# Performance work log

Measured on AMD Instinct MI355X. Metric: run time of the kernel, lower is better.

Reference implementation:

```python
import jax, jax.numpy as jnp
import numpy as np

N_NODES = 100000
N_EDGES = 600000
N_FEAT = 166
HID = 128


def _ln(x, g, b, eps=1e-5):
    m = x.mean(-1, keepdims=True)
    v = ((x - m) ** 2).mean(-1, keepdims=True)
    return (x - m) * jax.lax.rsqrt(v + eps) * g + b


def _gcn(h, row, col, em, W, b, n):
    # PyG GCNConv with add_self_loops=True; em is a 0/1 edge mask (recent/history split)
    hl = h @ W.T  # [N,H], PyG internal Linear has no bias
    deg = jax.ops.segment_sum(em, col, num_segments=n) + 1.0  # +1 for self loop
    dis = jax.lax.rsqrt(deg)
    coef = em * dis[row] * dis[col]
    agg = jax.ops.segment_sum(hl[row] * coef[:, None], col, num_segments=n)
    agg = agg + hl * (dis * dis)[:, None]  # self-loop message
    return agg + b


def setup_inputs():
    key = jax.random.key(0)
    ks = jax.random.split(key, 16)
    f32 = jnp.float32
    H = HID
    z = lambda *s: jnp.zeros(s, f32)
    nrm = lambda k, s, sc=0.05: jax.random.normal(k, s, f32) * sc
    return {
        "x": jax.random.normal(ks[0], (N_NODES, N_FEAT), f32),
        "edge_index": jax.random.randint(ks[1], (2, N_EDGES), 0, N_NODES, jnp.int32),
        "timestamps": jax.random.uniform(ks[2], (N_EDGES,), f32),
        "memory": nrm(ks[3], (N_NODES, H), 0.1),
        "W_in": nrm(ks[4], (H, N_FEAT)), "b_in": z(H),
        "W_time": nrm(ks[5], (H, 1)), "b_time": z(H),
        "W_ih": nrm(ks[6], (3 * H, H)), "W_hh": nrm(ks[7], (3 * H, H)),
        "b_ih": z(3 * H), "b_hh": z(3 * H),
        "W_gr": nrm(ks[8], (H, H)), "b_gr": z(H),
        "W_gh": nrm(ks[9], (H, H)), "b_gh": z(H),
        "ln_pa_g": jnp.ones((H,), f32), "ln_pa_b": z(H),
        "Wv": nrm(ks[10], (H, H)), "bv": z(H),
        "Wo": nrm(ks[11], (H, H)), "bo": z(H),
        "ln_at_g": jnp.ones((H,), f32), "ln_at_b": z(H),
        "W1": nrm(ks[12], (64, H)), "b1": z(64),
        "W2": nrm(ks[13], (2, 64)), "b2": z(2),
    }


def reference(x, edge_index, timestamps, memory, W_in, b_in, W_time, b_time,
              W_ih, W_hh, b_ih, b_hh, W_gr, b_gr, W_gh, b_gh,
              ln_pa_g, ln_pa_b, Wv, bv, Wo, bo, ln_at_g, ln_at_b,
              W1, b1, W2, b2):
    n = x.shape[0]
    row, col = edge_index[0], edge_index[1]
    # input projection + scatter-max temporal encoding
    h = x @ W_in.T + b_in
    nt = jnp.maximum(jax.ops.segment_max(timestamps, col, num_segments=n), 0.0)  # torch_scatter max inits at 0
    tmin, tmax = nt.min(), nt.max()
    nt = jnp.where(tmax > tmin, (nt - tmin) / (tmax - tmin + 1e-8), nt)
    h = h + nt[:, None] * W_time[:, 0] + b_time  # Linear(1, H)
    h = jax.nn.relu(h)
    h = h + memory
    # gather -> GRUCell -> scatter memory update for nodes touched by any edge
    upd = jnp.zeros((n,), bool).at[edge_index.reshape(-1)].set(True)
    gi = h @ W_ih.T + b_ih
    gh = memory @ W_hh.T + b_hh
    ir, iz, ic = jnp.split(gi, 3, axis=1)
    hr, hz, hc = jnp.split(gh, 3, axis=1)
    r = jax.nn.sigmoid(ir + hr)
    z = jax.nn.sigmoid(iz + hz)
    c = jnp.tanh(ic + r * hc)
    new_memory = jnp.where(upd[:, None], (1.0 - z) * c + z * memory, memory)
    # split edges by median timestamp, two GCN paths
    med = jnp.median(timestamps)
    m_rec = (timestamps >= med).astype(h.dtype)
    h_rec = _gcn(h, row, col, m_rec, W_gr, b_gr, n)
    h_his = _gcn(h, row, col, 1.0 - m_rec, W_gh, b_gh, n)
    # multi-path aggregation with softmax over per-path mean scores
    stacked = jnp.stack([h_rec, h_his], axis=1)  # [N,2,H]
    w = jax.nn.softmax(stacked.mean(-1), axis=-1)[..., None]
    h = _ln((stacked * w).sum(1), ln_pa_g, ln_pa_b)
    # anomaly attention: L=S=1 per "batch" element, so softmax over one key == 1
    # => attended = out_proj(v_proj(x)); query path cancels exactly
    attended = (h @ Wv.T + bv) @ Wo.T + bo
    h = _ln(h + attended, ln_at_g, ln_at_b)
    # classifier (eval mode: dropout = identity)
    logits = jax.nn.relu(h @ W1.T + b1) @ W2.T + b2
    return logits, new_memory
```

## Files before the change

### kernel.cpp

```cpp
#include <hip/hip_runtime.h>

#define NN 100000
#define NE 600000
#define NF 166
#define NH 128
#define NNH 12800000

enum { EPI_PLAIN = 0, EPI_RELU = 2, EPI_H = 3, EPI_HEAD = 4, EPI_ATTLN = 5 };

typedef short bf16x8 __attribute__((ext_vector_type(8)));
typedef float f32x16 __attribute__((ext_vector_type(16)));
typedef _Float16 f16x2 __attribute__((ext_vector_type(2)));
typedef _Float16 f16x4 __attribute__((ext_vector_type(4)));
typedef _Float16 f16x8 __attribute__((ext_vector_type(8)));

__device__ __forceinline__ unsigned short f2bf(float f) {
  unsigned u = __float_as_uint(f);
  u += 0x7fffu + ((u >> 16) & 1u);
  return (unsigned short)(u >> 16);
}

__device__ __forceinline__ unsigned short f2h(float f) {
  return __builtin_bit_cast(unsigned short, (_Float16)f);
}

__device__ __forceinline__ void gl_lds16(const void* g, void* l) {
  __builtin_amdgcn_global_load_lds((__attribute__((address_space(1))) void*)(void*)g,
                                   (__attribute__((address_space(3))) void*)l, 16, 0, 0);
}

template<int EPI, int OUTK, bool BIAS2, bool CONC, bool DUALA, bool F16, int NT>
__launch_bounds__(256)
__global__ void mgemm(const unsigned short* __restrict__ A, int lda,
                      const unsigned short* __restrict__ A2,
                      const unsigned short* __restrict__ W, int ldw,
                      float* __restrict__ C, int ldc,
                      unsigned short* __restrict__ Cb, int ldcb,
                      int K, int M,
                      const float* __restrict__ bias, const float* __restrict__ bias2,
                      const float* __restrict__ wtv, const float* __restrict__ ntv,
                      const float* __restrict__ mem, const int* __restrict__ scal)
{
  __shared__ unsigned short As[128 * 64];
  __shared__ unsigned short Bs[NT * 32 * 64];
  const int tid = threadIdx.x;
  const int wave = tid >> 6, lane = tid & 63;
  const int row0 = blockIdx.y * 128, col0 = blockIdx.x * NT * 32;
  if (DUALA && blockIdx.x) { A = A2; bias = bias2; }
  const int hi = lane >> 5, l5 = lane & 31, l3 = lane & 7;
  f32x16 acc[NT] = {};

  for (int k0 = 0; k0 < K; k0 += 64) {
    const unsigned short* Asrc = A;
    int kk = k0;
    if (CONC && k0 >= 128) { Asrc = A2; kk = k0 - 128; }
    __syncthreads();
#pragma unroll
    for (int q = 0; q < 4; ++q) {
      int id = q * 256 + tid;
      int r = id >> 3, cch = id & 7;
      int sw = ((cch ^ (r & 7)) << 3);
      int gr = row0 + r; if (gr > NN - 1) gr = NN - 1;
      gl_lds16(Asrc + (size_t)gr * lda + kk + sw, &As[(q * 256 + wave * 64) * 8]);
    }
#pragma unroll
    for (int q = 0; q < NT; ++q) {
      int id = q * 256 + tid;
      int r = id >> 3, cch = id & 7;
      int sw = ((cch ^ (r & 7)) << 3);
      int gm = col0 + r; if (gm > M - 1) gm = M - 1;
      gl_lds16(W + (size_t)gm * ldw + k0 + sw, &Bs[(q * 256 + wave * 64) * 8]);
    }
    __syncthreads();
#pragma unroll
    for (int s = 0; s < 4; ++s) {
      int slot8 = (((s * 2 + hi) ^ l3) << 3);
      bf16x8 a = *(const bf16x8*)&As[(wave * 32 + l5) * 64 + slot8];
#pragma unroll
      for (int t = 0; t < NT; ++t) {
        bf16x8 b = *(const bf16x8*)&Bs[(t * 32 + l5) * 64 + slot8];
        if (F16)
          acc[t] = __builtin_amdgcn_mfma_f32_32x32x16_f16(
              __builtin_bit_cast(f16x8, a), __builtin_bit_cast(f16x8, b), acc[t], 0, 0, 0);
        else
          acc[t] = __builtin_amdgcn_mfma_f32_32x32x16_bf16(a, b, acc[t], 0, 0, 0);
      }
    }
  }

  float tmin = 0.f, tmax = 0.f;
  if (EPI == EPI_H) { tmin = __int_as_float(scal[5]); tmax = __int_as_float(scal[6]); }
  float bc[NT], wc[NT], b2c[NT];
#pragma unroll
  for (int t = 0; t < NT; ++t) {
    int gcol = col0 + t * 32 + l5;
    int bcol = DUALA ? (gcol & 127) : gcol;
    bc[t] = bias ? bias[bcol] : 0.f;
    if (BIAS2) bc[t] += bias2[gcol];
    if (EPI == EPI_H)     { bc[t] += bias2[gcol]; wc[t] = wtv[gcol]; }
    if (EPI == EPI_ATTLN) { wc[t] = wtv[gcol]; b2c[t] = bias2[gcol]; }
  }
#pragma unroll
  for (int rg = 0; rg < 16; ++rg) {
    int lr = (rg & 3) + 8 * (rg >> 2) + 4 * hi;
    int grow = row0 + wave * 32 + lr;
    if (grow >= NN) continue;
    float ntn = 0.f;
    if (EPI == EPI_H) {
      ntn = ntv[grow];
      if (tmax > tmin) ntn = (ntn - tmin) / (tmax - tmin + 1e-8f);
    }
    float hv[NT];
#pragma unroll
    for (int t = 0; t < NT; ++t) {
      float v = acc[t][rg] + bc[t];
      if (EPI == EPI_RELU || EPI == EPI_HEAD) v = fmaxf(v, 0.f);
      if (EPI == EPI_H) {
        v += ntn * wc[t];
        v = fmaxf(v, 0.f);
        float mv = mem[(size_t)grow * NH + (col0 + t * 32 + l5)];
        v += mv;
        ((unsigned short*)C)[(size_t)grow * NH + (col0 + t * 32 + l5)] = f2bf(mv);
      }
      hv[t] = v;
    }
    if (EPI == EPI_ATTLN) {
      const _Float16* h2r = (const _Float16*)mem;
      float s = 0.f;
#pragma unroll
      for (int t = 0; t < NT; ++t) {
        hv[t] += (float)h2r[(size_t)grow * NH + (col0 + t * 32 + l5)];
        s += hv[t];
      }
#pragma unroll
      for (int d = 1; d < 32; d <<= 1) s += __shfl_xor(s, d);
      float mean = s * (1.f / 128.f);
      float var = 0.f;
#pragma unroll
      for (int t = 0; t < NT; ++t) { hv[t] -= mean; var += hv[t] * hv[t]; }
#pragma unroll
      for (int d = 1; d < 32; d <<= 1) var += __shfl_xor(var, d);
      float rstd = rsqrtf(var * (1.f / 128.f) + 1e-5f);
#pragma unroll
      for (int t = 0; t < NT; ++t) hv[t] = hv[t] * rstd * wc[t] + b2c[t];
    }
    if (EPI == EPI_HEAD) {
      float p0 = hv[0] * wtv[l5]      + hv[1] * wtv[32 + l5];
      float p1 = hv[0] * wtv[64 + l5] + hv[1] * wtv[96 + l5];
#pragma unroll
      for (int d = 1; d < 32; d <<= 1) { p0 += __shfl_xor(p0, d); p1 += __shfl_xor(p1, d); }
      if (l5 == 0) {
        C[(size_t)grow * 2]     = p0 + bias2[0];
        C[(size_t)grow * 2 + 1] = p1 + bias2[1];
      }
    } else {
#pragma unroll
      for (int t = 0; t < NT; ++t) {
        int gcol = col0 + t * 32 + l5;
        if (OUTK == 1) C[(size_t)grow * ldc + gcol] = hv[t];
        if (OUTK == 2) Cb[(size_t)grow * ldcb + gcol] = f2bf(hv[t]);
        if (OUTK == 3) Cb[(size_t)grow * ldcb + gcol] = f2h(hv[t]);
      }
    }
  }
}

__global__ void conv_x(const float* __restrict__ x, unsigned short* __restrict__ xb)
{
  int i = blockIdx.x * 256 + threadIdx.x;
  if (i >= NN * 192) return;
  int n = i / 192, c = i - n * 192;
  xb[i] = (c < NF) ? f2bf(x[n * NF + c]) : (unsigned short)0;
}

__global__ void conv_w(const float* __restrict__ Wi, const float* __restrict__ Wih,
                       const float* __restrict__ Whh, const float* __restrict__ Wgr,
                       const float* __restrict__ Wgh, const float* __restrict__ Wv,
                       const float* __restrict__ Wo, const float* __restrict__ W1,
                       unsigned short* __restrict__ wb)
{
  int i = blockIdx.x * 256 + threadIdx.x;
  if (i >= 196608) return;
  float v;
  if (i < 24576)       { int r = i / 192, c = i - r * 192; v = (c < NF) ? Wi[r * NF + c] : 0.f; }
  else if (i < 90112)  { int j = i - 24576; int r = j >> 8, c = j & 255;
                         v = (c < 128) ? Wih[r * 128 + c] : Whh[r * 128 + (c - 128)]; }
  else if (i < 122880) { int j = i - 90112; int r = j >> 7, c = j & 127;
                         v = (r < 128) ? Wih[(256 + r) * 128 + c] : Whh[(128 + r) * 128 + c]; }
  else if (i < 139264) v = Wgr[i - 122880];
  else if (i < 155648) v = Wgh[i - 139264];
  else if (i < 172032) v = Wv[i - 155648];
  else if (i < 188416) v = Wo[i - 172032];
  else                 v = W1[i - 188416];
  wb[i] = f2bf(v);
}

__global__ void compose_att(const float* __restrict__ Wv, const float* __restrict__ Wo,
                            const float* __restrict__ bv, const float* __restrict__ bo,
                            _Float16* __restrict__ wout, float* __restrict__ bout)
{
  int i = blockIdx.x * 256 + threadIdx.x;
  if (i >= 16384) return;
  int r = i >> 7, c = i & 127;
  float s = 0.f;
  for (int k = 0; k < 128; ++k) s = fmaf(Wo[r * 128 + k], Wv[k * 128 + c], s);
  wout[i] = (_Float16)s;
  if (c == 0) {
    float t = bo[r];
    for (int k = 0; k < 128; ++k) t = fmaf(Wo[r * 128 + k], bv[k], t);
    bout[r] = t;
  }
}

__device__ __forceinline__ int ts_bin(float t) {
  int b = (int)(t * 65536.0f);
  return b > 65535 ? 65535 : (b < 0 ? 0 : b);
}

__global__ void edge_pass1(const int* __restrict__ row, const int* __restrict__ col,
                           const float* __restrict__ ts,
                           float* nt, int* upd, int* cnt_all, int* hist1)
{
  int e = blockIdx.x * 256 + threadIdx.x;
  if (e >= NE) return;
  int r = row[e], c = col[e];
  float t = ts[e];
  atomicMax((int*)(nt + c), __float_as_int(t));
  upd[r] = 1; upd[c] = 1;
  atomicAdd(cnt_all + c, 1);
  atomicAdd(hist1 + ts_bin(t), 1);
}

__global__ void node_minmax(const float* __restrict__ nt, int* scal)
{
  int i = blockIdx.x * 256 + threadIdx.x;
  float v = (i < NN) ? nt[i] : nt[0];
  float vmin = v, vmax = v;
#pragma unroll
  for (int d = 1; d < 64; d <<= 1) {
    vmin = fminf(vmin, __shfl_xor(vmin, d));
    vmax = fmaxf(vmax, __shfl_xor(vmax, d));
  }
  __shared__ float smin[4], smax[4];
  int lane = threadIdx.x & 63, w = threadIdx.x >> 6;
  if (lane == 0) { smin[w] = vmin; smax[w] = vmax; }
  __syncthreads();
  if (threadIdx.x == 0) {
    float a = fminf(fminf(smin[0], smin[1]), fminf(smin[2], smin[3]));
    float b = fmaxf(fmaxf(smax[0], smax[1]), fmaxf(smax[2], smax[3]));
    atomicMin(scal + 5, __float_as_int(a));
    atomicMax(scal + 6, __float_as_int(b));
  }
}

__global__ void scan_hist1(const int* __restrict__ hist, int* scal)
{
  const int K1 = 299999, K2 = 300000;
  __shared__ int sums[256];
  __shared__ int pre[257];
  int t = threadIdx.x;
  int s = 0;
  for (int i = 0; i < 256; ++i) s += hist[t * 256 + i];
  sums[t] = s;
  __syncthreads();
  if (t == 0) { int run = 0; for (int i = 0; i < 256; ++i) { pre[i] = run; run += sums[i]; } pre[256] = run; }
  __syncthreads();
  int base = pre[t], nexts = base + sums[t];
  if (K1 >= base && K1 < nexts) {
    int run = base;
    for (int i = 0; i < 256; ++i) {
      int cv = hist[t * 256 + i];
      if (K1 < run + cv) { scal[0] = t * 256 + i; scal[1] = run; break; }
      run += cv;
    }
  }
  if (K2 >= base && K2 < nexts) {
    int run = base;
    for (int i = 0; i < 256; ++i) {
      int cv = hist[t * 256 + i];
      if (K2 < run + cv) { scal[2] = t * 256 + i; scal[3] = run; break; }
      run += cv;
    }
  }
}

#define CAND_CAP 4096
__global__ void collect_cand(const float* __restrict__ ts, const int* __restrict__ scal,
                             float* cand1, float* cand2, int* ccnt)
{
  int e = blockIdx.x * 256 + threadIdx.x;
  if (e >= NE) return;
  float t = ts[e];
  int b = ts_bin(t);
  if (b == scal[0]) {
    int s = atomicAdd(ccnt + 0, 1);
    if (s < CAND_CAP) cand1[s] = t;
  }
  if (b == scal[2]) {
    int s = atomicAdd(ccnt + 1, 1);
    if (s < CAND_CAP) cand2[s] = t;
  }
}

__global__ void select_med(const float* __restrict__ c1, const float* __restrict__ c2,
                           const int* __restrict__ ccnt, int* scal)
{
  __shared__ float res[2];
  for (int which = 0; which < 2; ++which) {
    const float* c = which ? c2 : c1;
    int m = ccnt[which]; if (m > CAND_CAP) m = CAND_CAP;
    int rank = which ? (300000 - scal[3]) : (299999 - scal[1]);
    for (int i = threadIdx.x; i < m; i += 256) {
      float v = c[i];
      int less = 0, eq = 0;
      for (int j = 0; j < m; ++j) { float w = c[j]; less += (w < v); eq += (w == v); }
      if (less <= rank && rank < less + eq) res[which] = v;
    }
  }
  __syncthreads();
  if (threadIdx.x == 0)
    ((float*)scal)[4] = 0.5f * (res[0] + res[1]);
}

__global__ void csr_scan1(const int* __restrict__ cnt, int* loc, int* bsum)
{
  __shared__ int s[256];
  int t = threadIdx.x;
  int i = blockIdx.x * 256 + t;
  int v = (i < NN) ? cnt[i] : 0;
  s[t] = v;
  __syncthreads();
  for (int d = 1; d < 256; d <<= 1) {
    int add = (t >= d) ? s[t - d] : 0;
    __syncthreads();
    s[t] += add;
    __syncthreads();
  }
  if (i < NN) loc[i] = s[t] - v;
  if (t == 255) bsum[blockIdx.x] = s[255];
}

__global__ void csr_scan2(int* bsum, int nb)
{
  if (threadIdx.x == 0) {
    int run = 0;
    for (int i = 0; i < nb; ++i) { int v = bsum[i]; bsum[i] = run; run += v; }
  }
}

__global__ void csr_scan3(const int* __restrict__ loc, const int* __restrict__ bsum,
                          int* off, int* fillpos)
{
  int i = blockIdx.x * 256 + threadIdx.x;
  if (i < NN) {
    int o = loc[i] + bsum[i >> 8];
    off[i] = o;
    fillpos[i] = o;
  }
  if (i == 0) off[NN] = NE;
}

__global__ void csr_fill(const int* __restrict__ row, const int* __restrict__ col,
                         const float* __restrict__ ts, const int* __restrict__ scal,
                         int* fillpos, int* elist, int* cnt_rec)
{
  int e = blockIdx.x * 256 + threadIdx.x;
  if (e >= NE) return;
  int c = col[e], r = row[e];
  int rec = (ts[e] >= __int_as_float(scal[4])) ? 1 : 0;
  if (rec) atomicAdd(cnt_rec + c, 1);
  int slot = atomicAdd(fillpos + c, 1);
  elist[slot] = r | (rec << 31);
}

__global__ void node_dis(const int* __restrict__ cnt_all, const int* __restrict__ cnt_rec,
                         float* dr, float* dh)
{
  int n = blockIdx.x * 256 + threadIdx.x;
  if (n >= NN) return;
  int ca = cnt_all[n], cr = cnt_rec[n];
  dr[n] = rsqrtf((float)cr + 1.f);
  dh[n] = rsqrtf((float)(ca - cr) + 1.f);
}

__device__ __forceinline__ float gru1(float rp, float zp, float ic, float hc, float mv) {
  float r = 1.f / (1.f + expf(-rp));
  float z = 1.f / (1.f + expf(-zp));
  float c = tanhf(ic + r * hc);
  return (1.f - z) * c + z * mv;
}

__global__ void gru_kernel(const _Float16* __restrict__ RZ, const _Float16* __restrict__ ICHC,
                           const float* __restrict__ mem, const int* __restrict__ upd,
                           float* __restrict__ out)
{
  int idx = blockIdx.x * 256 + threadIdx.x;
  if (idx >= NN * 32) return;
  int n = idx >> 5, q = (idx & 31) << 2;
  size_t p128 = (size_t)n * 128 + q;
  size_t p256 = (size_t)n * 256 + q;
  float4 mv = *(const float4*)(mem + p128);
  float4 o = mv;
  if (upd[n]) {
    f16x4 rp = *(const f16x4*)(RZ + p256);
    f16x4 zp = *(const f16x4*)(RZ + p256 + 128);
    f16x4 ic = *(const f16x4*)(ICHC + p256);
    f16x4 hc = *(const f16x4*)(ICHC + p256 + 128);
    o.x = gru1((float)rp[0], (float)zp[0], (float)ic[0], (float)hc[0], mv.x);
    o.y = gru1((float)rp[1], (float)zp[1], (float)ic[1], (float)hc[1], mv.y);
    o.z = gru1((float)rp[2], (float)zp[2], (float)ic[2], (float)hc[2], mv.z);
    o.w = gru1((float)rp[3], (float)zp[3], (float)ic[3], (float)hc[3], mv.w);
  }
  *(float4*)(out + p128) = o;
}

__global__ void gather_combine(const int* __restrict__ off, const int* __restrict__ elist,
                               const float* __restrict__ dis_r, const float* __restrict__ dis_h,
                               const _Float16* __restrict__ hl2,
                               const float* __restrict__ bgr, const float* __restrict__ bgh,
                               const float* __restrict__ g, const float* __restrict__ b,
                               _Float16* __restrict__ h2)
{
  int n = blockIdx.x * 4 + (threadIdx.x >> 6);
  if (n >= NN) return;
  int lane = threadIdx.x & 63;
  int o0 = __builtin_amdgcn_readfirstlane(off[n]);
  int o1 = __builtin_amdgcn_readfirstlane(off[n + 1]);
  float dnr = dis_r[n], dnh = dis_h[n];
  float arx = 0.f, ary = 0.f, ahx = 0.f, ahy = 0.f;
  int j = o0;
  for (; j + 1 < o1; j += 2) {
    int p0 = __builtin_amdgcn_readfirstlane(elist[j]);
    int p1 = __builtin_amdgcn_readfirstlane(elist[j + 1]);
    int r0 = p0 & 0x7fffffff, r1 = p1 & 0x7fffffff;
    int c0 = ((unsigned)p0) >> 31, c1 = ((unsigned)p1) >> 31;
    float d0 = c0 ? dis_r[r0] : dis_h[r0];
    float d1 = c1 ? dis_r[r1] : dis_h[r1];
    f16x2 v0 = *(const f16x2*)(hl2 + (size_t)r0 * 256 + ((c0 ^ 1) << 7) + (lane << 1));
    f16x2 v1 = *(const f16x2*)(hl2 + (size_t)r1 * 256 + ((c1 ^ 1) << 7) + (lane << 1));
    float k0 = d0 * (c0 ? dnr : dnh);
    float k1 = d1 * (c1 ? dnr : dnh);
    if (c0) { arx = fmaf(k0, (float)v0[0], arx); ary = fmaf(k0, (float)v0[1], ary); }
    else    { ahx = fmaf(k0, (float)v0[0], ahx); ahy = fmaf(k0, (float)v0[1], ahy); }
    if (c1) { arx = fmaf(k1, (float)v1[0], arx); ary = fmaf(k1, (float)v1[1], ary); }
    else    { ahx = fmaf(k1, (float)v1[0], ahx); ahy = fmaf(k1, (float)v1[1], ahy); }
  }
  if (j < o1) {
    int p0 = __builtin_amdgcn_readfirstlane(elist[j]);
    int r0 = p0 & 0x7fffffff;
    int c0 = ((unsigned)p0) >> 31;
    float d0 = c0 ? dis_r[r0] : dis_h[r0];
    f16x2 v0 = *(const f16x2*)(hl2 + (size_t)r0 * 256 + ((c0 ^ 1) << 7) + (lane << 1));
    float k0 = d0 * (c0 ? dnr : dnh);
    if (c0) { arx = fmaf(k0, (float)v0[0], arx); ary = fmaf(k0, (float)v0[1], ary); }
    else    { ahx = fmaf(k0, (float)v0[0], ahx); ahy = fmaf(k0, (float)v0[1], ahy); }
  }
  f16x2 lr = *(const f16x2*)(hl2 + (size_t)n * 256 + (lane << 1));
  f16x2 lh = *(const f16x2*)(hl2 + (size_t)n * 256 + 128 + (lane << 1));
  float2 br = *(const float2*)(bgr + (lane << 1));
  float2 bh = *(const float2*)(bgh + (lane << 1));
  float rx = arx + (float)lr[0] * dnr * dnr + br.x;
  float ry = ary + (float)lr[1] * dnr * dnr + br.y;
  float hx = ahx + (float)lh[0] * dnh * dnh + bh.x;
  float hy = ahy + (float)lh[1] * dnh * dnh + bh.y;
  float sa = rx + ry, sc = hx + hy;
#pragma unroll
  for (int d = 1; d < 64; d <<= 1) { sa += __shfl_xor(sa, d); sc += __shfl_xor(sc, d); }
  float m0 = sa * (1.f / 128.f), m1 = sc * (1.f / 128.f);
  float mx = fmaxf(m0, m1);
  float e0 = expf(m0 - mx), e1 = expf(m1 - mx);
  float inv = 1.f / (e0 + e1);
  float w0 = e0 * inv, w1 = e1 * inv;
  float yx = w0 * rx + w1 * hx;
  float yy = w0 * ry + w1 * hy;
  float s = yx + yy;
#pragma unroll
  for (int d = 1; d < 64; d <<= 1) s += __shfl_xor(s, d);
  float mean = s * (1.f / 128.f);
  float dx = yx - mean, dy = yy - mean;
  float vv = dx * dx + dy * dy;
#pragma unroll
  for (int d = 1; d < 64; d <<= 1) vv += __shfl_xor(vv, d);
  float rstd = rsqrtf(vv * (1.f / 128.f) + 1e-5f);
  float2 gg = *(const float2*)(g + (lane << 1));
  float2 bb = *(const float2*)(b + (lane << 1));
  f16x2 o;
  o[0] = (_Float16)(dx * rstd * gg.x + bb.x);
  o[1] = (_Float16)(dy * rstd * gg.y + bb.y);
  *(f16x2*)(h2 + (size_t)n * NH + (lane << 1)) = o;
}

extern "C" void kernel_launch(void* const* d_in, const int* in_sizes, int n_in,
                              void* d_out, int out_size, void* d_ws, size_t ws_size,
                              hipStream_t stream)
{
  const float* x      = (const float*)d_in[0];
  const int*   ei     = (const int*)  d_in[1];
  const float* ts     = (const float*)d_in[2];
  const float* mem    = (const float*)d_in[3];
  const float* W_in   = (const float*)d_in[4];
  const float* b_in   = (const float*)d_in[5];
  const float* W_time = (const float*)d_in[6];
  const float* b_time = (const float*)d_in[7];
  const float* W_ih   = (const float*)d_in[8];
  const float* W_hh   = (const float*)d_in[9];
  const float* b_ih   = (const float*)d_in[10];
  const float* b_hh   = (const float*)d_in[11];
  const float* W_gr   = (const float*)d_in[12];
  const float* b_gr   = (const float*)d_in[13];
  const float* W_gh   = (const float*)d_in[14];
  const float* b_gh   = (const float*)d_in[15];
  const float* ln_pa_g= (const float*)d_in[16];
  const float* ln_pa_b= (const float*)d_in[17];
  const float* Wv     = (const float*)d_in[18];
  const float* bv     = (const float*)d_in[19];
  const float* Wo     = (const float*)d_in[20];
  const float* bo     = (const float*)d_in[21];
  const float* ln_at_g= (const float*)d_in[22];
  const float* ln_at_b= (const float*)d_in[23];
  const float* W1     = (const float*)d_in[24];
  const float* b1     = (const float*)d_in[25];
  const float* W2     = (const float*)d_in[26];
  const float* b2     = (const float*)d_in[27];

  const int* row = ei;
  const int* col = ei + NE;
  float* out_logits = (float*)d_out;
  float* out_mem    = (float*)d_out + NN * 2;

  float* ws = (float*)d_ws;
  unsigned short* hb   = (unsigned short*)(ws);
  _Float16* h2         = (_Float16*)(ws);
  unsigned short* xb   = (unsigned short*)(ws + 6400000);
  _Float16* rz         = (_Float16*)(ws + 6400000);
  unsigned short* rb   = (unsigned short*)(ws + 6400000);
  _Float16* ichc       = (_Float16*)(ws + 19200000);
  _Float16* hl2        = (_Float16*)(ws + 32000000);
  unsigned short* memb = (unsigned short*)(ws + 44800000);
  unsigned short* wb   = (unsigned short*)(ws + 51200000);
  float* nt            = ws + 51350000;
  float* dis_r         = ws + 51450000;
  float* dis_h         = ws + 51550000;
  int* cnt_all         = (int*)(ws + 51650000);
  int* cnt_rec         = (int*)(ws + 51750000);
  int* upd             = (int*)(ws + 51850000);
  int* scal            = (int*)(ws + 51950000);
  float* batt          = ws + 51960000;
  float* cand1         = ws + 51970000;
  float* cand2         = ws + 51980000;
  int* ccnt            = (int*)(ws + 51990000);
  int* hist1           = (int*)(ws + 52000000);
  int* off             = (int*)(ws + 52100000);
  int* fillpos         = (int*)(ws + 52250000);
  int* loc             = (int*)(ws + 52400000);
  int* bsum            = (int*)(ws + 52550000);
  int* elist           = (int*)(ws + 52600000);

  unsigned short* wb_in = wb;
  unsigned short* wb_rz = wb + 24576;
  unsigned short* wb_c  = wb + 90112;
  unsigned short* wb_gr = wb + 122880;
  unsigned short* wb_o  = wb + 172032;
  unsigned short* wb_1  = wb + 188416;

  hipMemsetAsync(nt,      0, NN * 4, stream);
  hipMemsetAsync(cnt_all, 0, NN * 4, stream);
  hipMemsetAsync(cnt_rec, 0, NN * 4, stream);
  hipMemsetAsync(upd,     0, NN * 4, stream);
  hipMemsetAsync(hist1,   0, 65536 * 4, stream);
  hipMemsetAsync(scal,    0, 16 * 4, stream);
  hipMemsetAsync(scal + 5,0x7f, 4, stream);
  hipMemsetAsync(ccnt,    0, 8, stream);

  const int eb  = (NE + 255) / 256;
  const int nb  = (NN + 255) / 256;
  dim3 blk(256);
  const unsigned gy = (NN + 127) / 128;

  edge_pass1  <<<eb, 256, 0, stream>>>(row, col, ts, nt, upd, cnt_all, hist1);
  node_minmax <<<nb, 256, 0, stream>>>(nt, scal);
  scan_hist1  <<<1, 256, 0, stream>>>(hist1, scal);
  collect_cand<<<eb, 256, 0, stream>>>(ts, scal, cand1, cand2, ccnt);
  select_med  <<<1, 256, 0, stream>>>(cand1, cand2, ccnt, scal);

  conv_w     <<<768, 256, 0, stream>>>(W_in, W_ih, W_hh, W_gr, W_gh, Wv, Wo, W1, wb);
  compose_att<<<64, 256, 0, stream>>>(Wv, Wo, bv, bo, (_Float16*)wb_o, batt);
  conv_x     <<<75000, 256, 0, stream>>>(x, xb);

  mgemm<EPI_H, 2, false, false, false, false, 4><<<dim3(1, gy), blk, 0, stream>>>(
      xb, 192, nullptr, wb_in, 192, (float*)memb, 0, hb, NH, 192, 128,
      b_in, b_time, W_time, nt, mem, scal);
  mgemm<EPI_PLAIN, 3, true, true, false, false, 8><<<dim3(1, gy), blk, 0, stream>>>(
      hb, NH, memb, wb_rz, 256, nullptr, 0, (unsigned short*)rz, 256, 256, 256,
      b_ih, b_hh, nullptr, nullptr, nullptr, nullptr);
  mgemm<EPI_PLAIN, 3, false, false, true, false, 4><<<dim3(2, gy), blk, 0, stream>>>(
      hb, NH, memb, wb_c, NH, nullptr, 0, (unsigned short*)ichc, 256, 128, 256,
      b_ih + 256, b_hh + 256, nullptr, nullptr, nullptr, nullptr);
  gru_kernel<<<(NN * 32) / 256, 256, 0, stream>>>(rz, ichc, mem, upd, out_mem);

  csr_scan1<<<nb, 256, 0, stream>>>(cnt_all, loc, bsum);
  csr_scan2<<<1, 64, 0, stream>>>(bsum, nb);
  csr_scan3<<<nb, 256, 0, stream>>>(loc, bsum, off, fillpos);
  csr_fill <<<eb, 256, 0, stream>>>(row, col, ts, scal, fillpos, elist, cnt_rec);
  node_dis <<<nb, 256, 0, stream>>>(cnt_all, cnt_rec, dis_r, dis_h);

  mgemm<EPI_PLAIN, 3, false, false, false, false, 8><<<dim3(1, gy), blk, 0, stream>>>(
      hb, NH, nullptr, wb_gr, NH, nullptr, 0, (unsigned short*)hl2, 256, 128, 256,
      nullptr, nullptr, nullptr, nullptr, nullptr, nullptr);

  gather_combine<<<(NN + 3) / 4, 256, 0, stream>>>(off, elist, dis_r, dis_h, hl2,
      b_gr, b_gh, ln_pa_g, ln_pa_b, h2);

  mgemm<EPI_ATTLN, 2, false, false, false, true, 4><<<dim3(1, gy), blk, 0, stream>>>(
      (const unsigned short*)h2, NH, nullptr, wb_o, NH, nullptr, 0, rb, NH, 128, 128,
      batt, ln_at_b, ln_at_g, nullptr, (const float*)h2, scal);

  mgemm<EPI_HEAD, 0, false, false, false, false, 2><<<dim3(1, gy), blk, 0, stream>>>(
      rb, NH, nullptr, wb_1, NH, out_logits, 0, nullptr, 0, 128, 64,
      b1, b2, W2, nullptr, nullptr, nullptr);

  (void)in_sizes; (void)n_in; (void)out_size; (void)ws_size;
}
```

Baseline: 758.2 us.

## Restructure edge preprocessing around CSR with block-local histograms and per-node scan

Replaces the 65536-bin global-atomic timestamp histogram with a 1024-bin histogram that each block builds in shared memory and writes out as a partial, reduced in one scan kernel. Median-candidate collection moves into the CSR fill pass, which also stores timestamps in CSR order. A new node_scan kernel then derives per-node max time, recent-edge counts, degree normalisers, the recent flag bits and the min/max reduction from the CSR segments. This removes several global-atomic passes and separate kernels. The coarser bins put more candidates into the quadratic select_med step. The upd flag array shrinks to bytes.

```diff
diff --git a/kernel.cpp b/kernel.cpp
--- a/kernel.cpp
+++ b/kernel.cpp
@@ -212,96 +212,56 @@
   }
 }
 
+#define NBIN 1024
+#define HBLK 256
 __device__ __forceinline__ int ts_bin(float t) {
-  int b = (int)(t * 65536.0f);
-  return b > 65535 ? 65535 : (b < 0 ? 0 : b);
-}
-
-__global__ void edge_pass1(const int* __restrict__ row, const int* __restrict__ col,
+  int b = (int)(t * (float)NBIN);
+  return b > NBIN - 1 ? NBIN - 1 : (b < 0 ? 0 : b);
+}
+
+__global__ void edge_count(const int* __restrict__ row, const int* __restrict__ col,
                            const float* __restrict__ ts,
-                           float* nt, int* upd, int* cnt_all, int* hist1)
-{
-  int e = blockIdx.x * 256 + threadIdx.x;
-  if (e >= NE) return;
-  int r = row[e], c = col[e];
-  float t = ts[e];
-  atomicMax((int*)(nt + c), __float_as_int(t));
-  upd[r] = 1; upd[c] = 1;
-  atomicAdd(cnt_all + c, 1);
-  atomicAdd(hist1 + ts_bin(t), 1);
-}
-
-__global__ void node_minmax(const float* __restrict__ nt, int* scal)
-{
-  int i = blockIdx.x * 256 + threadIdx.x;
-  float v = (i < NN) ? nt[i] : nt[0];
-  float vmin = v, vmax = v;
-#pragma unroll
-  for (int d = 1; d < 64; d <<= 1) {
-    vmin = fminf(vmin, __shfl_xor(vmin, d));
-    vmax = fmaxf(vmax, __shfl_xor(vmax, d));
-  }
-  __shared__ float smin[4], smax[4];
-  int lane = threadIdx.x & 63, w = threadIdx.x >> 6;
-  if (lane == 0) { smin[w] = vmin; smax[w] = vmax; }
+                           int* __restrict__ cnt_all, unsigned char* __restrict__ upd,
+                           int* __restrict__ hpart)
+{
+  __shared__ unsigned hist[NBIN];
+  for (int i = threadIdx.x; i < NBIN; i += 256) hist[i] = 0;
   __syncthreads();
-  if (threadIdx.x == 0) {
-    float a = fminf(fminf(smin[0], smin[1]), fminf(smin[2], smin[3]));
-    float b = fmaxf(fmaxf(smax[0], smax[1]), fmaxf(smax[2], smax[3]));
-    atomicMin(scal + 5, __float_as_int(a));
-    atomicMax(scal + 6, __float_as_int(b));
-  }
-}
-
-__global__ void scan_hist1(const int* __restrict__ hist, int* scal)
-{
-  const int K1 = 299999, K2 = 300000;
-  __shared__ int sums[256];
-  __shared__ int pre[257];
+  for (int e = blockIdx.x * 256 + threadIdx.x; e < NE; e += 256 * HBLK) {
+    int c = col[e];
+    float t = ts[e];
+    atomicAdd(cnt_all + c, 1);
+    upd[row[e]] = 1;
+    atomicAdd(&hist[ts_bin(t)], 1u);
+  }
+  __syncthreads();
+  for (int i = threadIdx.x; i < NBIN; i += 256)
+    hpart[blockIdx.x * NBIN + i] = (int)hist[i];
+}
+
+__global__ void scan_hist(const int* __restrict__ hpart, int* scal)
+{
+  __shared__ int tot[NBIN];
   int t = threadIdx.x;
-  int s = 0;
-  for (int i = 0; i < 256; ++i) s += hist[t * 256 + i];
-  sums[t] = s;
+  for (int b = t; b < NBIN; b += 256) {
+    int s = 0;
+    for (int p = 0; p < HBLK; ++p) s += hpart[p * NBIN + b];
+    tot[b] = s;
+  }
   __syncthreads();
-  if (t == 0) { int run = 0; for (int i = 0; i < 256; ++i) { pre[i] = run; run += sums[i]; } pre[256] = run; }
-  __syncthreads();
-  int base = pre[t], nexts = base + sums[t];
-  if (K1 >= base && K1 < nexts) {
-    int run = base;
-    for (int i = 0; i < 256; ++i) {
-      int cv = hist[t * 256 + i];
-      if (K1 < run + cv) { scal[0] = t * 256 + i; scal[1] = run; break; }
-      run += cv;
-    }
-  }
-  if (K2 >= base && K2 < nexts) {
-    int run = base;
-    for (int i = 0; i < 256; ++i) {
-      int cv = hist[t * 256 + i];
-      if (K2 < run + cv) { scal[2] = t * 256 + i; scal[3] = run; break; }
-      run += cv;
+  if (t == 0) {
+    const int K1 = 299999, K2 = 300000;
+    int run = 0;
+    for (int b = 0; b < NBIN; ++b) {
+      int c = tot[b];
+      if (K1 >= run && K1 < run + c) { scal[0] = b; scal[1] = run; }
+      if (K2 >= run && K2 < run + c) { scal[2] = b; scal[3] = run; }
+      run += c;
     }
   }
 }
 
 #define CAND_CAP 4096
-__global__ void collect_cand(const float* __restrict__ ts, const int* __restrict__ scal,
-                             float* cand1, float* cand2, int* ccnt)
-{
-  int e = blockIdx.x * 256 + threadIdx.x;
-  if (e >= NE) return;
-  float t = ts[e];
-  int b = ts_bin(t);
-  if (b == scal[0]) {
-    int s = atomicAdd(ccnt + 0, 1);
-    if (s < CAND_CAP) cand1[s] = t;
-  }
-  if (b == scal[2]) {
-    int s = atomicAdd(ccnt + 1, 1);
-    if (s < CAND_CAP) cand2[s] = t;
-  }
-}
-
 __global__ void select_med(const float* __restrict__ c1, const float* __restrict__ c2,
                            const int* __restrict__ ccnt, int* scal)
 {
@@ -362,25 +322,67 @@
 
 __global__ void csr_fill(const int* __restrict__ row, const int* __restrict__ col,
                          const float* __restrict__ ts, const int* __restrict__ scal,
-                         int* fillpos, int* elist, int* cnt_rec)
+                         int* fillpos, int* __restrict__ elist, float* __restrict__ tsl,
+                         float* cand1, float* cand2, int* ccnt)
 {
   int e = blockIdx.x * 256 + threadIdx.x;
   if (e >= NE) return;
   int c = col[e], r = row[e];
-  int rec = (ts[e] >= __int_as_float(scal[4])) ? 1 : 0;
-  if (rec) atomicAdd(cnt_rec + c, 1);
+  float t = ts[e];
   int slot = atomicAdd(fillpos + c, 1);
-  elist[slot] = r | (rec << 31);
-}
-
-__global__ void node_dis(const int* __restrict__ cnt_all, const int* __restrict__ cnt_rec,
-                         float* dr, float* dh)
+  elist[slot] = r;
+  tsl[slot] = t;
+  int b = ts_bin(t);
+  if (b == scal[0]) {
+    int s = atomicAdd(ccnt + 0, 1);
+    if (s < CAND_CAP) cand1[s] = t;
+  }
+  if (b == scal[2]) {
+    int s = atomicAdd(ccnt + 1, 1);
+    if (s < CAND_CAP) cand2[s] = t;
+  }
+}
+
+__global__ void node_scan(const int* __restrict__ off, int* __restrict__ elist,
+                          const float* __restrict__ tsl, const int* __restrict__ scal,
+                          float* __restrict__ nt, float* __restrict__ dis_r,
+                          float* __restrict__ dis_h, unsigned char* __restrict__ upd,
+                          int* scal_mm)
 {
   int n = blockIdx.x * 256 + threadIdx.x;
-  if (n >= NN) return;
-  int ca = cnt_all[n], cr = cnt_rec[n];
-  dr[n] = rsqrtf((float)cr + 1.f);
-  dh[n] = rsqrtf((float)(ca - cr) + 1.f);
+  float mx = 0.f;
+  bool valid = n < NN;
+  if (valid) {
+    int o0 = off[n], o1 = off[n + 1];
+    float med = __int_as_float(scal[4]);
+    int cr = 0;
+    for (int j = o0; j < o1; ++j) {
+      float t = tsl[j];
+      mx = fmaxf(mx, t);
+      if (t >= med) { cr++; elist[j] |= 0x80000000; }
+    }
+    nt[n] = mx;
+    dis_r[n] = rsqrtf((float)cr + 1.f);
+    dis_h[n] = rsqrtf((float)(o1 - o0 - cr) + 1.f);
+    if (o1 > o0) upd[n] = 1;
+  }
+  float vmin = valid ? mx : 1e30f;
+  float vmax = valid ? mx : -1e30f;
+#pragma unroll
+  for (int d = 1; d < 64; d <<= 1) {
+    vmin = fminf(vmin, __shfl_xor(vmin, d));
+    vmax = fmaxf(vmax, __shfl_xor(vmax, d));
+  }
+  __shared__ float smin[4], smax[4];
+  int lane = threadIdx.x & 63, w = threadIdx.x >> 6;
+  if (lane == 0) { smin[w] = vmin; smax[w] = vmax; }
+  __syncthreads();
+  if (threadIdx.x == 0) {
+    float a = fminf(fminf(smin[0], smin[1]), fminf(smin[2], smin[3]));
+    float b = fmaxf(fmaxf(smax[0], smax[1]), fmaxf(smax[2], smax[3]));
+    atomicMin(scal_mm + 5, __float_as_int(a));
+    atomicMax(scal_mm + 6, __float_as_int(b));
+  }
 }
 
 __device__ __forceinline__ float gru1(float rp, float zp, float ic, float hc, float mv) {
@@ -391,7 +393,7 @@
 }
 
 __global__ void gru_kernel(const _Float16* __restrict__ RZ, const _Float16* __restrict__ ICHC,
-                           const float* __restrict__ mem, const int* __restrict__ upd,
+                           const float* __restrict__ mem, const unsigned char* __restrict__ upd,
                            float* __restrict__ out)
 {
   int idx = blockIdx.x * 256 + threadIdx.x;
@@ -542,19 +544,19 @@
   float* dis_r         = ws + 51450000;
   float* dis_h         = ws + 51550000;
   int* cnt_all         = (int*)(ws + 51650000);
-  int* cnt_rec         = (int*)(ws + 51750000);
-  int* upd             = (int*)(ws + 51850000);
+  unsigned char* upd   = (unsigned char*)(ws + 51850000);
   int* scal            = (int*)(ws + 51950000);
   float* batt          = ws + 51960000;
   float* cand1         = ws + 51970000;
   float* cand2         = ws + 51980000;
   int* ccnt            = (int*)(ws + 51990000);
-  int* hist1           = (int*)(ws + 52000000);
   int* off             = (int*)(ws + 52100000);
   int* fillpos         = (int*)(ws + 52250000);
   int* loc             = (int*)(ws + 52400000);
   int* bsum            = (int*)(ws + 52550000);
   int* elist           = (int*)(ws + 52600000);
+  float* tsl           = ws + 53200000;
+  int* hpart           = (int*)(ws + 53800000);
 
   unsigned short* wb_in = wb;
   unsigned short* wb_rz = wb + 24576;
@@ -563,11 +565,8 @@
   unsigned short* wb_o  = wb + 172032;
   unsigned short* wb_1  = wb + 188416;
 
-  hipMemsetAsync(nt,      0, NN * 4, stream);
   hipMemsetAsync(cnt_all, 0, NN * 4, stream);
-  hipMemsetAsync(cnt_rec, 0, NN * 4, stream);
-  hipMemsetAsync(upd,     0, NN * 4, stream);
-  hipMemsetAsync(hist1,   0, 65536 * 4, stream);
+  hipMemsetAsync(upd,     0, NN, stream);
   hipMemsetAsync(scal,    0, 16 * 4, stream);
   hipMemsetAsync(scal + 5,0x7f, 4, stream);
   hipMemsetAsync(ccnt,    0, 8, stream);
@@ -577,11 +576,16 @@
   dim3 blk(256);
   const unsigned gy = (NN + 127) / 128;
 
-  edge_pass1  <<<eb, 256, 0, stream>>>(row, col, ts, nt, upd, cnt_all, hist1);
-  node_minmax <<<nb, 256, 0, stream>>>(nt, scal);
-  scan_hist1  <<<1, 256, 0, stream>>>(hist1, scal);
-  collect_cand<<<eb, 256, 0, stream>>>(ts, scal, cand1, cand2, ccnt);
-  select_med  <<<1, 256, 0, stream>>>(cand1, cand2, ccnt, scal);
+  edge_count<<<HBLK, 256, 0, stream>>>(row, col, ts, cnt_all, upd, hpart);
+  scan_hist <<<1, 256, 0, stream>>>(hpart, scal);
+  csr_scan1 <<<nb, 256, 0, stream>>>(cnt_all, loc, bsum);
+  csr_scan2 <<<1, 64, 0, stream>>>(bsum, nb);
+  csr_scan3 <<<nb, 256, 0, stream>>>(loc, bsum, off, fillpos);
+  csr_fill  <<<eb, 256, 0, stream>>>(row, col, ts, scal, fillpos, elist, tsl,
+                                     cand1, cand2, ccnt);
+  select_med<<<1, 256, 0, stream>>>(cand1, cand2, ccnt, scal);
+  node_scan <<<nb, 256, 0, stream>>>(off, elist, tsl, scal, nt, dis_r, dis_h,
+                                     upd, scal);
 
   conv_w     <<<768, 256, 0, stream>>>(W_in, W_ih, W_hh, W_gr, W_gh, Wv, Wo, W1, wb);
   compose_att<<<64, 256, 0, stream>>>(Wv, Wo, bv, bo, (_Float16*)wb_o, batt);
@@ -598,12 +602,6 @@
       b_ih + 256, b_hh + 256, nullptr, nullptr, nullptr, nullptr);
   gru_kernel<<<(NN * 32) / 256, 256, 0, stream>>>(rz, ichc, mem, upd, out_mem);
 
-  csr_scan1<<<nb, 256, 0, stream>>>(cnt_all, loc, bsum);
-  csr_scan2<<<1, 64, 0, stream>>>(bsum, nb);
-  csr_scan3<<<nb, 256, 0, stream>>>(loc, bsum, off, fillpos);
-  csr_fill <<<eb, 256, 0, stream>>>(row, col, ts, scal, fillpos, elist, cnt_rec);
-  node_dis <<<nb, 256, 0, stream>>>(cnt_all, cnt_rec, dis_r, dis_h);
-
   mgemm<EPI_PLAIN, 3, false, false, false, false, 8><<<dim3(1, gy), blk, 0, stream>>>(
       hb, NH, nullptr, wb_gr, NH, nullptr, 0, (unsigned short*)hl2, 256, 128, 256,
       nullptr, nullptr, nullptr, nullptr, nullptr, nullptr);
```

After: 868.6 us. +14.6%, slower.
